# Optimization experiments

Hardware: AMD Instinct MI355X
Metric: run time of the kernel (lower is better)

## Reference

```python
import jax, jax.numpy as jnp
import numpy as np

PAD = 4          # displacement radius
WIN = 2 * PAD + 1  # 9 -> 81 displacement channels


def setup_inputs() -> dict:
    key = jax.random.key(0)
    k1, k2 = jax.random.split(key)
    B, C, H, W = 4, 128, 128, 256
    first = jax.random.normal(k1, (B, C, H, W), dtype=jnp.float32)
    second = jax.random.normal(k2, (B, C, H, W), dtype=jnp.float32)
    return {"first": first, "second": second}


def reference(first, second):
    """FlowNet-style correlation / cost volume.

    out[b, (p+4)*9 + (o+4), y, x] = mean_c first[b,c,y,x] * second_pad[b,c,y+p+4,x+o+4]
    with second zero-padded by 4 on each spatial side.
    """
    B, C, H, W = first.shape
    second_pad = jnp.pad(second, ((0, 0), (0, 0), (PAD, PAD), (PAD, PAD)))
    outs = []
    for p in range(WIN):        # vertical displacement index (p - 4)
        for o in range(WIN):    # horizontal displacement index (o - 4)
            shifted = second_pad[:, :, p:p + H, o:o + W]  # [B,C,H,W]
            outs.append(jnp.mean(first * shifted, axis=1))  # [B,H,W]
    return jnp.stack(outs, axis=1)  # [B,81,H,W]
```

## Files before the change

### kernel.cpp

```cpp
#include <hip/hip_runtime.h>
#include <hip/hip_bf16.h>


namespace {
constexpr int kC = 128, kH = 128, kW = 256;
constexpr int kWin = 9;
constexpr int kYB = 4, kXB = 32;
constexpr int kSR = kYB + 8;
constexpr int kSX = kXB + 16;
constexpr int kCP = 40;
constexpr int kKC = 32;
constexpr int kNK = kC / kKC;
constexpr int kSSz = kSR * kSX * kCP;
constexpr int kFSz = kYB * kXB * kCP;
constexpr int kBufSz = kSSz + kFSz;
constexpr int kSU = kSR * (kSX / 4) * (kKC / 8);
constexpr int kFU = kYB * (kXB / 4) * (kKC / 8);
constexpr int kTU = kSU + kFU;
constexpr int kThreads = 1024;
constexpr int kBlocks = 4 * (kH / kYB) * (kW / kXB);
constexpr int kOS = 132;
constexpr int kCStr = kH * kW;

typedef __attribute__((ext_vector_type(8))) short bf16x8;
typedef __attribute__((ext_vector_type(4))) float f32x4;
}

__global__ __launch_bounds__(kThreads) void corr_mfma(
    const float* __restrict__ first,
    const float* __restrict__ second,
    float* __restrict__ out)
{
    __shared__ __align__(16) unsigned short lds[kBufSz];

    const int tid  = threadIdx.x;
    const int lane = tid & 63;
    const int wid  = tid >> 6;
    const int yslot = wid >> 2;
    const int mn    = wid & 3;

    int bid = blockIdx.x;
    bid = (bid & 7) * (kBlocks / 8) + (bid >> 3);
    const int b   = bid >> 8;
    const int rem = bid & 255;
    const int y0  = (rem >> 3) * kYB;
    const int X0  = (rem & 7) * kXB;

    const float* ug = nullptr;
    int ul = -1;
    if (tid < kSU) {
        int co = tid & 3, xq = (tid >> 2) % 12, row = tid / 48;
        int yg = y0 - 4 + row, xg = X0 - 8 + xq * 4;
        ul = (row * kSX + xq * 4) * kCP + co * 8;
        if (yg >= 0 && yg < kH && xg >= 0 && xg <= kW - 4)
            ug = second + ((size_t)(b * kC + co * 8) * kH + yg) * kW + xg;
    } else if (tid < kTU) {
        int u2 = tid - kSU;
        int co = u2 & 3, xq = (u2 >> 2) & 7, row = u2 >> 5;
        ul = kSSz + (row * kXB + xq * 4) * kCP + co * 8;
        ug = first + ((size_t)(b * kC + co * 8) * kH + (y0 + row)) * kW
                   + (X0 + xq * 4);
    }

    float4 pv[8];
    auto issue = [&](int kc) {
        if (ul < 0) return;
        const float4 z = make_float4(0.f, 0.f, 0.f, 0.f);
#pragma unroll
        for (int j = 0; j < 8; ++j) pv[j] = z;
        if (ug) {
            const float* g = ug + (size_t)kc * kKC * kCStr;
#pragma unroll
            for (int j = 0; j < 8; ++j)
                pv[j] = *(const float4*)(g + (size_t)j * kCStr);
        }
    };
    auto write_lds = [&]() {
        if (ul < 0) return;
#pragma unroll
        for (int xi = 0; xi < 4; ++xi) {
            union { uint4 q; __hip_bfloat162 h[4]; } pk;
#pragma unroll
            for (int jj = 0; jj < 4; ++jj) {
                float lo = ((const float*)&pv[2 * jj])[xi];
                float hi = ((const float*)&pv[2 * jj + 1])[xi];
                pk.h[jj] = __float22bfloat162_rn(make_float2(lo, hi));
            }
            *(uint4*)&lds[ul + xi * kCP] = pk.q;
        }
    };

    const int l15 = lane & 15, lg = lane >> 4;
    const int Ms = mn >> 1, Ns = (mn + 1) >> 1;
    const int aoff = kSSz + (yslot * kXB + Ms * 16 + l15) * kCP + lg * 8;
    const int boff = (yslot * kSX + Ns * 16 + l15) * kCP + lg * 8;

    f32x4 acc[kWin];
    {
        f32x4 z = {0.f, 0.f, 0.f, 0.f};
#pragma unroll
        for (int p = 0; p < kWin; ++p) acc[p] = z;
    }

    issue(0);
    for (int kc = 0; kc < kNK; ++kc) {
        write_lds();
        if (kc < kNK - 1) issue(kc + 1);
        __syncthreads();
        bf16x8 a = *(const bf16x8*)&lds[aoff];
#pragma unroll
        for (int p = 0; p < kWin; ++p) {
            bf16x8 bb = *(const bf16x8*)&lds[boff + p * (kSX * kCP)];
            acc[p] = __builtin_amdgcn_mfma_f32_16x16x32_bf16(a, bb, acc[p], 0, 0, 0);
        }
        __syncthreads();
    }

    float* outb = (float*)lds;
    const float inv = 1.0f / (float)kC;
    const int delta = (mn & 1) ? 12 : -4;
#pragma unroll
    for (int p = 0; p < kWin; ++p) {
#pragma unroll
        for (int r = 0; r < 4; ++r) {
            int m = (lg << 2) + r;
            int o = l15 - m + delta;
            if (o >= 0 && o < kWin) {
                int d = p * kWin + o;
                outb[d * kOS + yslot * kXB + Ms * 16 + m] = acc[p][r] * inv;
            }
        }
    }
    __syncthreads();

    const size_t ob = (size_t)b * (kWin * kWin) * kCStr;
    for (int i = tid; i < kWin * kWin * kYB * (kXB / 4); i += kThreads) {
        int d = i >> 5;
        int r2 = i & 31;
        int yy = r2 >> 3, xq = r2 & 7;
        float4 v = *(const float4*)&outb[d * kOS + yy * kXB + xq * 4];
        *(float4*)&out[ob + ((size_t)d * kH + (y0 + yy)) * kW + X0 + xq * 4] = v;
    }
}

extern "C" void kernel_launch(void* const* d_in, const int* in_sizes, int n_in,
                              void* d_out, int out_size, void* d_ws, size_t ws_size,
                              hipStream_t stream) {
    const float* first  = (const float*)d_in[0];
    const float* second = (const float*)d_in[1];
    float* out = (float*)d_out;
    dim3 grid(kBlocks);
    dim3 block(kThreads);
    hipLaunchKernelGGL(corr_mfma, grid, block, 0, stream, first, second, out);
}
```

Baseline: 63.07 us.

## Double tile height and give each wave two MFMA column tiles

Doubles the block's row tile from 4 to 8 rows, which cuts the redundant halo rows of the second input loaded per block. Work is remapped so each wave owns one row and one 16-pixel half, holding two sets of nine accumulators that reuse a single A fragment across both B column tiles. The LDS channel pad shrinks to fit the larger tile, the global-load thread mapping is reordered for better coalescing, and the block-to-XCD swizzle is rewritten. Costs are higher register pressure from doubled accumulators and fewer blocks, which may reduce occupancy and parallelism.

```diff
diff --git a/kernel.cpp b/kernel.cpp
--- a/kernel.cpp
+++ b/kernel.cpp
@@ -5,21 +5,20 @@
 namespace {
 constexpr int kC = 128, kH = 128, kW = 256;
 constexpr int kWin = 9;
-constexpr int kYB = 4, kXB = 32;
+constexpr int kYB = 8, kXB = 32;
 constexpr int kSR = kYB + 8;
 constexpr int kSX = kXB + 16;
-constexpr int kCP = 40;
+constexpr int kCP = 36;
 constexpr int kKC = 32;
 constexpr int kNK = kC / kKC;
 constexpr int kSSz = kSR * kSX * kCP;
 constexpr int kFSz = kYB * kXB * kCP;
-constexpr int kBufSz = kSSz + kFSz;
 constexpr int kSU = kSR * (kSX / 4) * (kKC / 8);
 constexpr int kFU = kYB * (kXB / 4) * (kKC / 8);
-constexpr int kTU = kSU + kFU;
 constexpr int kThreads = 1024;
 constexpr int kBlocks = 4 * (kH / kYB) * (kW / kXB);
-constexpr int kOS = 132;
+constexpr int kOS = kYB * kXB + 4;
+constexpr int kLdsE = 81 * kOS * 2;
 constexpr int kCStr = kH * kW;
 
 typedef __attribute__((ext_vector_type(8))) short bf16x8;
@@ -31,52 +30,54 @@
     const float* __restrict__ second,
     float* __restrict__ out)
 {
-    __shared__ __align__(16) unsigned short lds[kBufSz];
+    __shared__ __align__(16) unsigned short lds[kLdsE];
 
     const int tid  = threadIdx.x;
     const int lane = tid & 63;
     const int wid  = tid >> 6;
-    const int yslot = wid >> 2;
-    const int mn    = wid & 3;
+    const int yw   = wid >> 1;
+    const int half = wid & 1;
 
-    int bid = blockIdx.x;
-    bid = (bid & 7) * (kBlocks / 8) + (bid >> 3);
-    const int b   = bid >> 8;
-    const int rem = bid & 255;
-    const int y0  = (rem >> 3) * kYB;
-    const int X0  = (rem & 7) * kXB;
+    const int bid = blockIdx.x;
+    const int xcd = bid & 7;
+    const int seq = bid >> 3;
+    const int xt  = seq & 7;
+    const int g   = ((seq >> 3) << 3) + xcd;
+    const int b   = g >> 4;
+    const int y0  = (g & 15) * kYB;
+    const int X0  = xt * kXB;
+
+    const size_t ibase = (size_t)b * kC * kCStr;
 
     const float* ug = nullptr;
-    int ul = -1;
+    int ul;
     if (tid < kSU) {
-        int co = tid & 3, xq = (tid >> 2) % 12, row = tid / 48;
+        int xq = tid % 12, co = (tid / 12) & 3, row = tid / 48;
         int yg = y0 - 4 + row, xg = X0 - 8 + xq * 4;
         ul = (row * kSX + xq * 4) * kCP + co * 8;
         if (yg >= 0 && yg < kH && xg >= 0 && xg <= kW - 4)
-            ug = second + ((size_t)(b * kC + co * 8) * kH + yg) * kW + xg;
-    } else if (tid < kTU) {
+            ug = second + ibase + (size_t)(co * 8) * kCStr + (size_t)yg * kW + xg;
+    } else {
         int u2 = tid - kSU;
-        int co = u2 & 3, xq = (u2 >> 2) & 7, row = u2 >> 5;
+        int xq = u2 & 7, co = (u2 >> 3) & 3, row = u2 >> 5;
         ul = kSSz + (row * kXB + xq * 4) * kCP + co * 8;
-        ug = first + ((size_t)(b * kC + co * 8) * kH + (y0 + row)) * kW
-                   + (X0 + xq * 4);
+        ug = first + ibase + (size_t)(co * 8) * kCStr
+                   + (size_t)(y0 + row) * kW + (X0 + xq * 4);
     }
 
     float4 pv[8];
     auto issue = [&](int kc) {
-        if (ul < 0) return;
         const float4 z = make_float4(0.f, 0.f, 0.f, 0.f);
 #pragma unroll
         for (int j = 0; j < 8; ++j) pv[j] = z;
         if (ug) {
-            const float* g = ug + (size_t)kc * kKC * kCStr;
+            const float* gp = ug + (size_t)kc * kKC * kCStr;
 #pragma unroll
             for (int j = 0; j < 8; ++j)
-                pv[j] = *(const float4*)(g + (size_t)j * kCStr);
+                pv[j] = *(const float4*)(gp + (size_t)j * kCStr);
         }
     };
     auto write_lds = [&]() {
-        if (ul < 0) return;
 #pragma unroll
         for (int xi = 0; xi < 4; ++xi) {
             union { uint4 q; __hip_bfloat162 h[4]; } pk;
@@ -91,15 +92,16 @@
     };
 
     const int l15 = lane & 15, lg = lane >> 4;
-    const int Ms = mn >> 1, Ns = (mn + 1) >> 1;
-    const int aoff = kSSz + (yslot * kXB + Ms * 16 + l15) * kCP + lg * 8;
-    const int boff = (yslot * kSX + Ns * 16 + l15) * kCP + lg * 8;
+    const int aoff  = kSSz + (yw * kXB + half * 16 + l15) * kCP + lg * 8;
+    const int boffB = (yw * kSX + half * 16 + l15) * kCP + lg * 8;
 
-    f32x4 acc[kWin];
+    f32x4 acc[2][kWin];
     {
         f32x4 z = {0.f, 0.f, 0.f, 0.f};
 #pragma unroll
-        for (int p = 0; p < kWin; ++p) acc[p] = z;
+        for (int j = 0; j < 2; ++j)
+#pragma unroll
+            for (int p = 0; p < kWin; ++p) acc[j][p] = z;
     }
 
     issue(0);
@@ -109,34 +111,40 @@
         __syncthreads();
         bf16x8 a = *(const bf16x8*)&lds[aoff];
 #pragma unroll
-        for (int p = 0; p < kWin; ++p) {
-            bf16x8 bb = *(const bf16x8*)&lds[boff + p * (kSX * kCP)];
-            acc[p] = __builtin_amdgcn_mfma_f32_16x16x32_bf16(a, bb, acc[p], 0, 0, 0);
-        }
+        for (int j = 0; j < 2; ++j)
+#pragma unroll
+            for (int p = 0; p < kWin; ++p) {
+                bf16x8 bb = *(const bf16x8*)
+                    &lds[boffB + j * (16 * kCP) + p * (kSX * kCP)];
+                acc[j][p] = __builtin_amdgcn_mfma_f32_16x16x32_bf16(
+                    a, bb, acc[j][p], 0, 0, 0);
+            }
         __syncthreads();
     }
 
     float* outb = (float*)lds;
     const float inv = 1.0f / (float)kC;
-    const int delta = (mn & 1) ? 12 : -4;
 #pragma unroll
-    for (int p = 0; p < kWin; ++p) {
+    for (int j = 0; j < 2; ++j) {
+        const int delta = j ? 12 : -4;
 #pragma unroll
-        for (int r = 0; r < 4; ++r) {
-            int m = (lg << 2) + r;
-            int o = l15 - m + delta;
-            if (o >= 0 && o < kWin) {
-                int d = p * kWin + o;
-                outb[d * kOS + yslot * kXB + Ms * 16 + m] = acc[p][r] * inv;
+        for (int p = 0; p < kWin; ++p)
+#pragma unroll
+            for (int r = 0; r < 4; ++r) {
+                int m = (lg << 2) + r;
+                int o = l15 - m + delta;
+                if (o >= 0 && o < kWin) {
+                    int d = p * kWin + o;
+                    outb[d * kOS + yw * kXB + half * 16 + m] = acc[j][p][r] * inv;
+                }
             }
-        }
     }
     __syncthreads();
 
     const size_t ob = (size_t)b * (kWin * kWin) * kCStr;
     for (int i = tid; i < kWin * kWin * kYB * (kXB / 4); i += kThreads) {
-        int d = i >> 5;
-        int r2 = i & 31;
+        int d = i >> 6;
+        int r2 = i & 63;
         int yy = r2 >> 3, xq = r2 & 7;
         float4 v = *(const float4*)&outb[d * kOS + yy * kXB + xq * 4];
         *(float4*)&out[ob + ((size_t)d * kH + (y0 + yy)) * kW + X0 + xq * 4] = v;
```

Measured after the change: 69.50 us. +10.2%, slower.

## Shrink tile to 16 columns with 512-thread blocks and new XCD-aware block mapping

Applied to the files above, without the earlier changes.

Halves the x-tile width to 16 columns and the block to 8 waves, so each wave computes one 16-wide M tile against two N halves. Block-to-tile remapping now groups blocks on the same XCD by y rows and batch while iterating x tiles sequentially. It adds launch_bounds occupancy hint of 4 blocks. Smaller tiles raise halo overhead (second tile is 32 wide for 16 outputs) but give more blocks and better occupancy.

```diff
diff --git a/kernel.cpp b/kernel.cpp
--- a/kernel.cpp
+++ b/kernel.cpp
@@ -5,7 +5,7 @@
 namespace {
 constexpr int kC = 128, kH = 128, kW = 256;
 constexpr int kWin = 9;
-constexpr int kYB = 4, kXB = 32;
+constexpr int kYB = 4, kXB = 16;
 constexpr int kSR = kYB + 8;
 constexpr int kSX = kXB + 16;
 constexpr int kCP = 40;
@@ -13,53 +13,57 @@
 constexpr int kNK = kC / kKC;
 constexpr int kSSz = kSR * kSX * kCP;
 constexpr int kFSz = kYB * kXB * kCP;
-constexpr int kBufSz = kSSz + kFSz;
+constexpr int kLdsE = kSSz + kFSz;
 constexpr int kSU = kSR * (kSX / 4) * (kKC / 8);
 constexpr int kFU = kYB * (kXB / 4) * (kKC / 8);
 constexpr int kTU = kSU + kFU;
-constexpr int kThreads = 1024;
+constexpr int kThreads = 512;
 constexpr int kBlocks = 4 * (kH / kYB) * (kW / kXB);
-constexpr int kOS = 132;
+constexpr int kOS = kYB * kXB + 4;
 constexpr int kCStr = kH * kW;
 
 typedef __attribute__((ext_vector_type(8))) short bf16x8;
 typedef __attribute__((ext_vector_type(4))) float f32x4;
 }
 
-__global__ __launch_bounds__(kThreads) void corr_mfma(
+__global__ __launch_bounds__(kThreads, 4) void corr_mfma(
     const float* __restrict__ first,
     const float* __restrict__ second,
     float* __restrict__ out)
 {
-    __shared__ __align__(16) unsigned short lds[kBufSz];
+    __shared__ __align__(16) unsigned short lds[kLdsE];
 
     const int tid  = threadIdx.x;
     const int lane = tid & 63;
     const int wid  = tid >> 6;
-    const int yslot = wid >> 2;
-    const int mn    = wid & 3;
+    const int yslot = wid >> 1;
+    const int Ns    = wid & 1;
 
-    int bid = blockIdx.x;
-    bid = (bid & 7) * (kBlocks / 8) + (bid >> 3);
-    const int b   = bid >> 8;
-    const int rem = bid & 255;
-    const int y0  = (rem >> 3) * kYB;
-    const int X0  = (rem & 7) * kXB;
+    const int bid = blockIdx.x;
+    const int xcd = bid & 7;
+    const int seq = bid >> 3;
+    const int xt  = seq & 15;
+    const int g   = ((seq >> 4) << 3) + xcd;
+    const int b   = g >> 5;
+    const int y0  = (g & 31) * kYB;
+    const int X0  = xt * kXB;
+
+    const size_t ibase = (size_t)b * kC * kCStr;
 
     const float* ug = nullptr;
     int ul = -1;
     if (tid < kSU) {
-        int co = tid & 3, xq = (tid >> 2) % 12, row = tid / 48;
+        int co = tid & 3, xq = (tid >> 2) & 7, row = tid >> 5;
         int yg = y0 - 4 + row, xg = X0 - 8 + xq * 4;
         ul = (row * kSX + xq * 4) * kCP + co * 8;
         if (yg >= 0 && yg < kH && xg >= 0 && xg <= kW - 4)
-            ug = second + ((size_t)(b * kC + co * 8) * kH + yg) * kW + xg;
+            ug = second + ibase + (size_t)(co * 8) * kCStr + (size_t)yg * kW + xg;
     } else if (tid < kTU) {
         int u2 = tid - kSU;
-        int co = u2 & 3, xq = (u2 >> 2) & 7, row = u2 >> 5;
+        int co = u2 & 3, xq = (u2 >> 2) & 3, row = u2 >> 4;
         ul = kSSz + (row * kXB + xq * 4) * kCP + co * 8;
-        ug = first + ((size_t)(b * kC + co * 8) * kH + (y0 + row)) * kW
-                   + (X0 + xq * 4);
+        ug = first + ibase + (size_t)(co * 8) * kCStr
+                   + (size_t)(y0 + row) * kW + (X0 + xq * 4);
     }
 
     float4 pv[8];
@@ -69,10 +73,10 @@
 #pragma unroll
         for (int j = 0; j < 8; ++j) pv[j] = z;
         if (ug) {
-            const float* g = ug + (size_t)kc * kKC * kCStr;
+            const float* gp = ug + (size_t)kc * kKC * kCStr;
 #pragma unroll
             for (int j = 0; j < 8; ++j)
-                pv[j] = *(const float4*)(g + (size_t)j * kCStr);
+                pv[j] = *(const float4*)(gp + (size_t)j * kCStr);
         }
     };
     auto write_lds = [&]() {
@@ -91,9 +95,8 @@
     };
 
     const int l15 = lane & 15, lg = lane >> 4;
-    const int Ms = mn >> 1, Ns = (mn + 1) >> 1;
-    const int aoff = kSSz + (yslot * kXB + Ms * 16 + l15) * kCP + lg * 8;
-    const int boff = (yslot * kSX + Ns * 16 + l15) * kCP + lg * 8;
+    const int aoff = kSSz + (yslot * kXB + l15) * kCP + lg * 8;
+    const int boff = ((yslot)*kSX + Ns * 16 + l15) * kCP + lg * 8;
 
     f32x4 acc[kWin];
     {
@@ -118,26 +121,25 @@
 
     float* outb = (float*)lds;
     const float inv = 1.0f / (float)kC;
-    const int delta = (mn & 1) ? 12 : -4;
+    const int delta = Ns ? 12 : -4;
 #pragma unroll
-    for (int p = 0; p < kWin; ++p) {
+    for (int p = 0; p < kWin; ++p)
 #pragma unroll
         for (int r = 0; r < 4; ++r) {
             int m = (lg << 2) + r;
             int o = l15 - m + delta;
             if (o >= 0 && o < kWin) {
                 int d = p * kWin + o;
-                outb[d * kOS + yslot * kXB + Ms * 16 + m] = acc[p][r] * inv;
+                outb[d * kOS + yslot * kXB + m] = acc[p][r] * inv;
             }
         }
-    }
     __syncthreads();
 
     const size_t ob = (size_t)b * (kWin * kWin) * kCStr;
     for (int i = tid; i < kWin * kWin * kYB * (kXB / 4); i += kThreads) {
-        int d = i >> 5;
-        int r2 = i & 31;
-        int yy = r2 >> 3, xq = r2 & 7;
+        int d  = i >> 4;
+        int r2 = i & 15;
+        int yy = r2 >> 2, xq = r2 & 3;
         float4 v = *(const float4*)&outb[d * kOS + yy * kXB + xq * 4];
         *(float4*)&out[ob + ((size_t)d * kH + (y0 + yy)) * kW + X0 + xq * 4] = v;
     }
```

New measurement: 63.86 us. No clear change (+1.3%).
